# Performance work log

Hardware: AMD Instinct MI355X
Metric: run time of the kernel (lower is better)

## Reference

```python
import jax, jax.numpy as jnp
import numpy as np

B, F, S, H = 1024, 64, 512, 128


def setup_inputs() -> dict:
    key = jax.random.key(0)
    ks = jax.random.split(key, 9)
    x = jax.random.normal(ks[0], (B, F, S), dtype=jnp.float32)
    available_len = jax.random.randint(ks[1], (B,), 1, S // 2).astype(jnp.int32)
    extra = jax.random.randint(ks[2], (B,), 0, S // 2)
    predict_len = jnp.minimum(available_len + extra, S).astype(jnp.int32)
    s = 1.0 / float(np.sqrt(H))  # PyTorch default uniform init scale
    u = lambda k, shape: jax.random.uniform(k, shape, jnp.float32, -s, s)
    W_ih = u(ks[3], (4 * H, F))
    W_hh = u(ks[4], (4 * H, H))
    b_ih = u(ks[5], (4 * H,))
    b_hh = u(ks[6], (4 * H,))
    W_den = u(ks[7], (F, H))
    b_den = u(ks[8], (F,))
    init_ch = jnp.zeros((1, 2 * H), dtype=jnp.float32)  # nn.Parameter(zeros(1, 2*n_hidden))
    return {"x": x, "available_len": available_len, "predict_len": predict_len,
            "W_ih": W_ih, "W_hh": W_hh, "b_ih": b_ih, "b_hh": b_hh,
            "W_den": W_den, "b_den": b_den, "init_ch": init_ch}


def reference(x, available_len, predict_len, W_ih, W_hh, b_ih, b_hh, W_den, b_den, init_ch):
    """Masked autoregressive LSTMCell recurrence.

    Row r is active at step t iff t < predict_len[r]; once inactive it never
    re-activates (the torch code's per-step gather of c_1/h_1 by predict_len is
    exactly this monotone-shrinking active set, expressed here as a masked
    full-batch state update). For t >= available_len[r] (and still active) the
    input is the model's own previous prediction (auto-regression feedback).
    Returns the permuted buffer (seq_len, batch, n_fea), matching the torch code.
    """
    Bb, Ff, Ss = x.shape
    Hh = W_hh.shape[1]
    xs = jnp.transpose(x, (2, 0, 1))  # (S, B, F)
    c0 = jnp.broadcast_to(init_ch[:, :Hh], (Bb, Hh))
    h0 = jnp.broadcast_to(init_ch[:, Hh:], (Bb, Hh))

    def step(carry, inp):
        h, c, prev_out = carry
        t, x_t = inp  # t: scalar step index, x_t: (B, F)
        sel = t < predict_len                       # active rows
        use_pred = (t >= available_len) & sel
        inp_t = jnp.where(use_pred[:, None], prev_out, x_t)
        gates = inp_t @ W_ih.T + b_ih + h @ W_hh.T + b_hh  # (B, 4H)
        i, f, g, o = jnp.split(gates, 4, axis=-1)
        c_new = jax.nn.sigmoid(f) * c + jax.nn.sigmoid(i) * jnp.tanh(g)
        h_new = jax.nn.sigmoid(o) * jnp.tanh(c_new)
        h = jnp.where(sel[:, None], h_new, h)
        c = jnp.where(sel[:, None], c_new, c)
        pred = h_new @ W_den.T + b_den              # (B, F)
        out_t = jnp.where(sel[:, None], pred, inp_t)  # x[t, sel] <- prediction
        return (h, c, out_t), out_t

    _, ys = jax.lax.scan(step, (h0, c0, jnp.zeros_like(xs[0])),
                         (jnp.arange(Ss), xs))
    return ys  # (S, B, F)
```

## Files before the change

### kernel.cpp

```cpp
#include <hip/hip_runtime.h>

#define BB 1024
#define FF 64
#define SS 512
#define HH 128
#define ZP 200
#define ZROWS 16
#define OUTSTRIDE (BB*FF)

typedef __attribute__((ext_vector_type(8))) short bf16x8;
typedef __attribute__((ext_vector_type(4))) float f32x4;

__device__ __forceinline__ unsigned short f2bf(float f) {
    unsigned int u = __float_as_uint(f);
    u += 0x7fff + ((u >> 16) & 1);
    return (unsigned short)(u >> 16);
}

__device__ __forceinline__ void bar_lds() {
    asm volatile("s_waitcnt lgkmcnt(0)" ::: "memory");
    __builtin_amdgcn_s_barrier();
    __builtin_amdgcn_sched_barrier(0);
}

__global__ __launch_bounds__(512)
void lstm_mfma_kernel(const float* __restrict__ x,
                      const int* __restrict__ available_len,
                      const int* __restrict__ predict_len,
                      const float* __restrict__ W_ih,
                      const float* __restrict__ W_hh,
                      const float* __restrict__ b_ih,
                      const float* __restrict__ b_hh,
                      const float* __restrict__ W_den,
                      const float* __restrict__ b_den,
                      const float* __restrict__ init_ch,
                      float* __restrict__ out)
{
    const int b0  = blockIdx.x * 4;
    const int tid = threadIdx.x;
    const int w   = tid >> 6;
    const int l   = tid & 63;
    const int l16 = l & 15;
    const int lq  = l >> 4;
    const bool w4 = (w < 4);

    __shared__ __align__(16) unsigned short zbuf[2][ZROWS * ZP];

    for (int i = tid; i < 2 * ZROWS * ZP / 2; i += 512)
        ((unsigned int*)zbuf)[i] = 0u;

    const int p0 = predict_len[b0], p1 = predict_len[b0+1],
              p2 = predict_len[b0+2], p3 = predict_len[b0+3];
    const int maxP  = max(max(p0, p1), max(p2, p3));
    const int P_my  = predict_len[b0 + lq];
    const int AV_my = available_len[b0 + lq];

    bf16x8 wg[4][6];
    float bias[4];
    #pragma unroll
    for (int g = 0; g < 4; ++g) {
        const int n = 128*g + 16*w + l16;
        const float* rih = W_ih + n * FF;
        const float* rhh = W_hh + n * HH;
        #pragma unroll
        for (int kt = 0; kt < 6; ++kt) {
            const int k = 32*kt + 8*lq;
            const float* src = (k < 64) ? (rih + k) : (rhh + (k - 64));
            bf16x8 r;
            #pragma unroll
            for (int i = 0; i < 8; i++) r[i] = (short)f2bf(src[i]);
            wg[g][kt] = r;
        }
        bias[g] = b_ih[n] + b_hh[n];
    }

    bf16x8 wd0, wd1, wd2, wd3;
    float bden = 0.f;
    size_t xbase = 0;
    int AV_x = 0;
    if (w4) {
        const int f = 16*w + l16;
        const float* rd = W_den + f * HH;
        bf16x8 r;
        #pragma unroll
        for (int i = 0; i < 8; i++) r[i] = (short)f2bf(rd[0*32 + 8*lq + i]);
        wd0 = r;
        #pragma unroll
        for (int i = 0; i < 8; i++) r[i] = (short)f2bf(rd[1*32 + 8*lq + i]);
        wd1 = r;
        #pragma unroll
        for (int i = 0; i < 8; i++) r[i] = (short)f2bf(rd[2*32 + 8*lq + i]);
        wd2 = r;
        #pragma unroll
        for (int i = 0; i < 8; i++) r[i] = (short)f2bf(rd[3*32 + 8*lq + i]);
        wd3 = r;
        bden = b_den[f];
        xbase = ((size_t)(b0 + w) * FF + l) * SS;
        AV_x  = available_len[b0 + w];
    }

    const int unit  = 16*w + l16;
    const int abase = l16*ZP + 8*lq;
    float c = init_ch[unit];
    const float h0v = init_ch[HH + unit];
    float* outb = out + (size_t)(b0 + lq) * FF + 16*w + l16;

    bar_lds();

    zbuf[0][(4*lq)*ZP + 64 + unit] = f2bf(h0v);
    if (w4) zbuf[0][(4*w)*ZP + l] = f2bf(x[xbase]);

    float4 qc = {0.f,0.f,0.f,0.f};
    if (w4 && AV_x > 1) qc = *(const float4*)(x + xbase);

    int cur = 0;

#define DO_STEP(S, XNEXT)                                                      \
  do {                                                                         \
    const int s_ = (S);                                                        \
    bar_lds();                                               \
    const unsigned short* zc_ = zbuf[cur];                                     \
    bf16x8 a0 = *(const bf16x8*)(zc_ + abase +   0);                           \
    bf16x8 a1 = *(const bf16x8*)(zc_ + abase +  32);                           \
    bf16x8 a2 = *(const bf16x8*)(zc_ + abase +  64);                           \
    bf16x8 a3 = *(const bf16x8*)(zc_ + abase +  96);                           \
    bf16x8 a4 = *(const bf16x8*)(zc_ + abase + 128);                           \
    bf16x8 a5 = *(const bf16x8*)(zc_ + abase + 160);                           \
    f32x4 ac0 = {0.f,0.f,0.f,0.f}, ac1 = {0.f,0.f,0.f,0.f},                    \
          ac2 = {0.f,0.f,0.f,0.f}, ac3 = {0.f,0.f,0.f,0.f};                    \
    ac0 = __builtin_amdgcn_mfma_f32_16x16x32_bf16(a0, wg[0][0], ac0, 0,0,0);   \
    ac1 = __builtin_amdgcn_mfma_f32_16x16x32_bf16(a0, wg[1][0], ac1, 0,0,0);   \
    ac2 = __builtin_amdgcn_mfma_f32_16x16x32_bf16(a0, wg[2][0], ac2, 0,0,0);   \
    ac3 = __builtin_amdgcn_mfma_f32_16x16x32_bf16(a0, wg[3][0], ac3, 0,0,0);   \
    ac0 = __builtin_amdgcn_mfma_f32_16x16x32_bf16(a1, wg[0][1], ac0, 0,0,0);   \
    ac1 = __builtin_amdgcn_mfma_f32_16x16x32_bf16(a1, wg[1][1], ac1, 0,0,0);   \
    ac2 = __builtin_amdgcn_mfma_f32_16x16x32_bf16(a1, wg[2][1], ac2, 0,0,0);   \
    ac3 = __builtin_amdgcn_mfma_f32_16x16x32_bf16(a1, wg[3][1], ac3, 0,0,0);   \
    ac0 = __builtin_amdgcn_mfma_f32_16x16x32_bf16(a2, wg[0][2], ac0, 0,0,0);   \
    ac1 = __builtin_amdgcn_mfma_f32_16x16x32_bf16(a2, wg[1][2], ac1, 0,0,0);   \
    ac2 = __builtin_amdgcn_mfma_f32_16x16x32_bf16(a2, wg[2][2], ac2, 0,0,0);   \
    ac3 = __builtin_amdgcn_mfma_f32_16x16x32_bf16(a2, wg[3][2], ac3, 0,0,0);   \
    ac0 = __builtin_amdgcn_mfma_f32_16x16x32_bf16(a3, wg[0][3], ac0, 0,0,0);   \
    ac1 = __builtin_amdgcn_mfma_f32_16x16x32_bf16(a3, wg[1][3], ac1, 0,0,0);   \
    ac2 = __builtin_amdgcn_mfma_f32_16x16x32_bf16(a3, wg[2][3], ac2, 0,0,0);   \
    ac3 = __builtin_amdgcn_mfma_f32_16x16x32_bf16(a3, wg[3][3], ac3, 0,0,0);   \
    ac0 = __builtin_amdgcn_mfma_f32_16x16x32_bf16(a4, wg[0][4], ac0, 0,0,0);   \
    ac1 = __builtin_amdgcn_mfma_f32_16x16x32_bf16(a4, wg[1][4], ac1, 0,0,0);   \
    ac2 = __builtin_amdgcn_mfma_f32_16x16x32_bf16(a4, wg[2][4], ac2, 0,0,0);   \
    ac3 = __builtin_amdgcn_mfma_f32_16x16x32_bf16(a4, wg[3][4], ac3, 0,0,0);   \
    ac0 = __builtin_amdgcn_mfma_f32_16x16x32_bf16(a5, wg[0][5], ac0, 0,0,0);   \
    ac1 = __builtin_amdgcn_mfma_f32_16x16x32_bf16(a5, wg[1][5], ac1, 0,0,0);   \
    ac2 = __builtin_amdgcn_mfma_f32_16x16x32_bf16(a5, wg[2][5], ac2, 0,0,0);   \
    ac3 = __builtin_amdgcn_mfma_f32_16x16x32_bf16(a5, wg[3][5], ac3, 0,0,0);   \
    const float g0 = ac0[0] + bias[0];                                         \
    const float g1 = ac1[0] + bias[1];                                         \
    const float g2 = ac2[0] + bias[2];                                         \
    const float g3 = ac3[0] + bias[3];                                         \
    const float si = 1.f / (1.f + __expf(-g0));                                \
    const float sf = 1.f / (1.f + __expf(-g1));                                \
    const float tg = 1.f - 2.f / (__expf(2.f * g2) + 1.f);                     \
    const float so = 1.f / (1.f + __expf(-g3));                                \
    const float cn = sf * c + si * tg;                                         \
    const float tc = 1.f - 2.f / (__expf(2.f * cn) + 1.f);                     \
    const float hn = so * tc;                                                  \
    const int nxt_ = cur ^ 1;                                                  \
    if (s_ < P_my) { c = cn; zbuf[nxt_][(4*lq)*ZP + 64 + unit] = f2bf(hn); }   \
    bar_lds();                                                \
    if (w4) {                                                                  \
      const unsigned short* zn_ = zbuf[nxt_];                                  \
      bf16x8 h0f = *(const bf16x8*)(zn_ + abase + 64 +  0);                    \
      bf16x8 h1f = *(const bf16x8*)(zn_ + abase + 64 + 32);                    \
      bf16x8 h2f = *(const bf16x8*)(zn_ + abase + 64 + 64);                    \
      bf16x8 h3f = *(const bf16x8*)(zn_ + abase + 64 + 96);                    \
      f32x4 pa = {0.f,0.f,0.f,0.f}, pb = {0.f,0.f,0.f,0.f};                    \
      pa = __builtin_amdgcn_mfma_f32_16x16x32_bf16(h0f, wd0, pa, 0,0,0);       \
      pb = __builtin_amdgcn_mfma_f32_16x16x32_bf16(h2f, wd2, pb, 0,0,0);       \
      pa = __builtin_amdgcn_mfma_f32_16x16x32_bf16(h1f, wd1, pa, 0,0,0);       \
      pb = __builtin_amdgcn_mfma_f32_16x16x32_bf16(h3f, wd3, pb, 0,0,0);       \
      const float pred_ = pa[0] + pb[0] + bden;                                \
      if (s_ < P_my) {                                                         \
        outb[(size_t)s_ * OUTSTRIDE] = pred_;                                  \
        if (s_ + 1 >= AV_my)                                                   \
          zbuf[nxt_][(4*lq)*ZP + 16*w + l16] = f2bf(pred_);                    \
      }                                                                        \
      if (s_ + 1 < AV_x) zbuf[nxt_][(4*w)*ZP + l] = f2bf(XNEXT);               \
    }                                                                          \
    cur = nxt_;                                                                \
  } while (0)

    int t4 = 0;
    for (; t4 + 4 <= maxP; t4 += 4) {
        float4 qn = {0.f,0.f,0.f,0.f};
        if (w4 && (t4 + 4 < AV_x))
            qn = *(const float4*)(x + xbase + t4 + 4);
        DO_STEP(t4 + 0, qc.y);
        DO_STEP(t4 + 1, qc.z);
        DO_STEP(t4 + 2, qc.w);
        DO_STEP(t4 + 3, qn.x);
        qc = qn;
    }
    for (; t4 < maxP; ++t4) {
        float xs = 0.f;
        if (w4 && (t4 + 1 < AV_x)) xs = x[xbase + t4 + 1];
        DO_STEP(t4, xs);
    }
#undef DO_STEP
}

__global__ void tail_copy(const float* __restrict__ x,
                          const int* __restrict__ predict_len,
                          float* __restrict__ out)
{
    __shared__ float tile[64][65];
    const int b  = blockIdx.x;
    const int t0 = blockIdx.y * 64;
    const int P  = predict_len[b];
    if (t0 + 64 <= P) return;

    const int tid = threadIdx.x;
    const int tt  = tid & 63;
    const int fb  = tid >> 6;
    #pragma unroll
    for (int i = 0; i < 16; i++) {
        int f = fb * 16 + i;
        tile[f][tt] = x[(size_t)b * FF * SS + (size_t)f * SS + t0 + tt];
    }
    __syncthreads();
    const int f2 = tid & 63;
    const int tb = tid >> 6;
    #pragma unroll
    for (int i = 0; i < 16; i++) {
        int tloc = tb * 16 + i;
        int t    = t0 + tloc;
        if (t >= P) out[(size_t)t * BB * FF + (size_t)b * FF + f2] = tile[f2][tloc];
    }
}

extern "C" void kernel_launch(void* const* d_in, const int* in_sizes, int n_in,
                              void* d_out, int out_size, void* d_ws, size_t ws_size,
                              hipStream_t stream) {
    const float* x       = (const float*)d_in[0];
    const int*   avail   = (const int*)  d_in[1];
    const int*   plen    = (const int*)  d_in[2];
    const float* W_ih    = (const float*)d_in[3];
    const float* W_hh    = (const float*)d_in[4];
    const float* b_ih    = (const float*)d_in[5];
    const float* b_hh    = (const float*)d_in[6];
    const float* W_den   = (const float*)d_in[7];
    const float* b_den   = (const float*)d_in[8];
    const float* init_ch = (const float*)d_in[9];
    float*       out     = (float*)d_out;

    tail_copy<<<dim3(BB, SS/64), dim3(256), 0, stream>>>(x, plen, out);
    lstm_mfma_kernel<<<dim3(BB/4), dim3(512), 0, stream>>>(
        x, avail, plen, W_ih, W_hh, b_ih, b_hh, W_den, b_den, init_ch, out);
}
```

Baseline: 487.5 us.

## Pack 16 batch rows per block to fill MFMA M dimension

Each block now processes 16 batch rows instead of 4, so all four accumulator rows of every 16x16 MFMA tile carry useful data instead of zero padding. The cell update, predictions and x staging loop over four rows per lane, and every wave now loads x for two rows. The launch shrinks to a quarter of the blocks, which leaves most CUs idle. Each serial step also does four times the elementwise work, which may lengthen the latency-bound recurrence.

```diff
diff --git a/kernel.cpp b/kernel.cpp
--- a/kernel.cpp
+++ b/kernel.cpp
@@ -5,8 +5,7 @@
 #define SS 512
 #define HH 128
 #define ZP 200
-#define ZROWS 16
-#define OUTSTRIDE (BB*FF)
+#define OUTS (BB*FF)
 
 typedef __attribute__((ext_vector_type(8))) short bf16x8;
 typedef __attribute__((ext_vector_type(4))) float f32x4;
@@ -36,7 +35,7 @@
                       const float* __restrict__ init_ch,
                       float* __restrict__ out)
 {
-    const int b0  = blockIdx.x * 4;
+    const int b0  = blockIdx.x * 16;
     const int tid = threadIdx.x;
     const int w   = tid >> 6;
     const int l   = tid & 63;
@@ -44,16 +43,21 @@
     const int lq  = l >> 4;
     const bool w4 = (w < 4);
 
-    __shared__ __align__(16) unsigned short zbuf[2][ZROWS * ZP];
-
-    for (int i = tid; i < 2 * ZROWS * ZP / 2; i += 512)
+    __shared__ __align__(16) unsigned short zbuf[2][16 * ZP];
+
+    for (int i = tid; i < 2 * 16 * ZP / 2; i += 512)
         ((unsigned int*)zbuf)[i] = 0u;
 
-    const int p0 = predict_len[b0], p1 = predict_len[b0+1],
-              p2 = predict_len[b0+2], p3 = predict_len[b0+3];
-    const int maxP  = max(max(p0, p1), max(p2, p3));
-    const int P_my  = predict_len[b0 + lq];
-    const int AV_my = available_len[b0 + lq];
+    int maxP = 1;
+    #pragma unroll
+    for (int i = 0; i < 16; i++) maxP = max(maxP, predict_len[b0 + i]);
+
+    int Pv[4], Av[4];
+    #pragma unroll
+    for (int r = 0; r < 4; r++) {
+        Pv[r] = predict_len[b0 + 4*lq + r];
+        Av[r] = available_len[b0 + 4*lq + r];
+    }
 
     bf16x8 wg[4][6];
     float bias[4];
@@ -76,8 +80,6 @@
 
     bf16x8 wd0, wd1, wd2, wd3;
     float bden = 0.f;
-    size_t xbase = 0;
-    int AV_x = 0;
     if (w4) {
         const int f = 16*w + l16;
         const float* rd = W_den + f * HH;
@@ -95,30 +97,39 @@
         for (int i = 0; i < 8; i++) r[i] = (short)f2bf(rd[3*32 + 8*lq + i]);
         wd3 = r;
         bden = b_den[f];
-        xbase = ((size_t)(b0 + w) * FF + l) * SS;
-        AV_x  = available_len[b0 + w];
-    }
+    }
+
+    const size_t xb1 = ((size_t)(b0 + w)     * FF + l) * SS;
+    const size_t xb2 = ((size_t)(b0 + w + 8) * FF + l) * SS;
+    const int AX1 = available_len[b0 + w];
+    const int AX2 = available_len[b0 + w + 8];
 
     const int unit  = 16*w + l16;
     const int abase = l16*ZP + 8*lq;
-    float c = init_ch[unit];
-    const float h0v = init_ch[HH + unit];
-    float* outb = out + (size_t)(b0 + lq) * FF + 16*w + l16;
+    float cc[4];
+    const float c0v = init_ch[unit];
+    #pragma unroll
+    for (int r = 0; r < 4; r++) cc[r] = c0v;
+    const unsigned short h0b = f2bf(init_ch[HH + unit]);
+    float* outp = out + (size_t)(b0 + 4*lq) * FF + 16*w + l16;
 
     bar_lds();
 
-    zbuf[0][(4*lq)*ZP + 64 + unit] = f2bf(h0v);
-    if (w4) zbuf[0][(4*w)*ZP + l] = f2bf(x[xbase]);
-
-    float4 qc = {0.f,0.f,0.f,0.f};
-    if (w4 && AV_x > 1) qc = *(const float4*)(x + xbase);
+    #pragma unroll
+    for (int r = 0; r < 4; r++) zbuf[0][(4*lq + r)*ZP + 64 + unit] = h0b;
+    zbuf[0][w*ZP + l]       = f2bf(x[xb1]);
+    zbuf[0][(w + 8)*ZP + l] = f2bf(x[xb2]);
+
+    float4 q1 = {0.f,0.f,0.f,0.f}, q2 = {0.f,0.f,0.f,0.f};
+    if (AX1 > 1) q1 = *(const float4*)(x + xb1);
+    if (AX2 > 1) q2 = *(const float4*)(x + xb2);
 
     int cur = 0;
 
-#define DO_STEP(S, XNEXT)                                                      \
+#define DO_STEP(S, XN1, XN2)                                                   \
   do {                                                                         \
     const int s_ = (S);                                                        \
-    bar_lds();                                               \
+    bar_lds();                                                         \
     const unsigned short* zc_ = zbuf[cur];                                     \
     bf16x8 a0 = *(const bf16x8*)(zc_ + abase +   0);                           \
     bf16x8 a1 = *(const bf16x8*)(zc_ + abase +  32);                           \
@@ -152,19 +163,27 @@
     ac1 = __builtin_amdgcn_mfma_f32_16x16x32_bf16(a5, wg[1][5], ac1, 0,0,0);   \
     ac2 = __builtin_amdgcn_mfma_f32_16x16x32_bf16(a5, wg[2][5], ac2, 0,0,0);   \
     ac3 = __builtin_amdgcn_mfma_f32_16x16x32_bf16(a5, wg[3][5], ac3, 0,0,0);   \
-    const float g0 = ac0[0] + bias[0];                                         \
-    const float g1 = ac1[0] + bias[1];                                         \
-    const float g2 = ac2[0] + bias[2];                                         \
-    const float g3 = ac3[0] + bias[3];                                         \
-    const float si = 1.f / (1.f + __expf(-g0));                                \
-    const float sf = 1.f / (1.f + __expf(-g1));                                \
-    const float tg = 1.f - 2.f / (__expf(2.f * g2) + 1.f);                     \
-    const float so = 1.f / (1.f + __expf(-g3));                                \
-    const float cn = sf * c + si * tg;                                         \
-    const float tc = 1.f - 2.f / (__expf(2.f * cn) + 1.f);                     \
-    const float hn = so * tc;                                                  \
     const int nxt_ = cur ^ 1;                                                  \
-    if (s_ < P_my) { c = cn; zbuf[nxt_][(4*lq)*ZP + 64 + unit] = f2bf(hn); }   \
+    _Pragma("unroll")                                                          \
+    for (int r = 0; r < 4; r++) {                                              \
+      const float g0 = ac0[r] + bias[0];                                       \
+      const float g1 = ac1[r] + bias[1];                                       \
+      const float g2 = ac2[r] + bias[2];                                       \
+      const float g3 = ac3[r] + bias[3];                                       \
+      const float si = 1.f / (1.f + __expf(-g0));                              \
+      const float sf = 1.f / (1.f + __expf(-g1));                              \
+      const float tg = 1.f - 2.f / (__expf(2.f * g2) + 1.f);                   \
+      const float so = 1.f / (1.f + __expf(-g3));                              \
+      const float cn = sf * cc[r] + si * tg;                                   \
+      const float tc = 1.f - 2.f / (__expf(2.f * cn) + 1.f);                   \
+      const float hn = so * tc;                                                \
+      if (s_ < Pv[r]) {                                                        \
+        cc[r] = cn;                                                            \
+        zbuf[nxt_][(4*lq + r)*ZP + 64 + unit] = f2bf(hn);                      \
+      }                                                                        \
+    }                                                                          \
+    if (s_ + 1 < AX1) zbuf[nxt_][w*ZP + l]       = f2bf(XN1);                  \
+    if (s_ + 1 < AX2) zbuf[nxt_][(w + 8)*ZP + l] = f2bf(XN2);                  \
     bar_lds();                                                \
     if (w4) {                                                                  \
       const unsigned short* zn_ = zbuf[nxt_];                                  \
@@ -177,32 +196,35 @@
       pb = __builtin_amdgcn_mfma_f32_16x16x32_bf16(h2f, wd2, pb, 0,0,0);       \
       pa = __builtin_amdgcn_mfma_f32_16x16x32_bf16(h1f, wd1, pa, 0,0,0);       \
       pb = __builtin_amdgcn_mfma_f32_16x16x32_bf16(h3f, wd3, pb, 0,0,0);       \
-      const float pred_ = pa[0] + pb[0] + bden;                                \
-      if (s_ < P_my) {                                                         \
-        outb[(size_t)s_ * OUTSTRIDE] = pred_;                                  \
-        if (s_ + 1 >= AV_my)                                                   \
-          zbuf[nxt_][(4*lq)*ZP + 16*w + l16] = f2bf(pred_);                    \
+      _Pragma("unroll")                                                        \
+      for (int r = 0; r < 4; r++) {                                            \
+        if (s_ < Pv[r]) {                                                      \
+          const float pred_ = pa[r] + pb[r] + bden;                            \
+          outp[(size_t)s_ * OUTS + r * FF] = pred_;                            \
+          if (s_ + 1 >= Av[r])                                                 \
+            zbuf[nxt_][(4*lq + r)*ZP + 16*w + l16] = f2bf(pred_);              \
+        }                                                                      \
       }                                                                        \
-      if (s_ + 1 < AV_x) zbuf[nxt_][(4*w)*ZP + l] = f2bf(XNEXT);               \
     }                                                                          \
     cur = nxt_;                                                                \
   } while (0)
 
     int t4 = 0;
     for (; t4 + 4 <= maxP; t4 += 4) {
-        float4 qn = {0.f,0.f,0.f,0.f};
-        if (w4 && (t4 + 4 < AV_x))
-            qn = *(const float4*)(x + xbase + t4 + 4);
-        DO_STEP(t4 + 0, qc.y);
-        DO_STEP(t4 + 1, qc.z);
-        DO_STEP(t4 + 2, qc.w);
-        DO_STEP(t4 + 3, qn.x);
-        qc = qn;
+        float4 qn1 = {0.f,0.f,0.f,0.f}, qn2 = {0.f,0.f,0.f,0.f};
+        if (t4 + 4 < AX1) qn1 = *(const float4*)(x + xb1 + t4 + 4);
+        if (t4 + 4 < AX2) qn2 = *(const float4*)(x + xb2 + t4 + 4);
+        DO_STEP(t4 + 0, q1.y, q2.y);
+        DO_STEP(t4 + 1, q1.z, q2.z);
+        DO_STEP(t4 + 2, q1.w, q2.w);
+        DO_STEP(t4 + 3, qn1.x, qn2.x);
+        q1 = qn1; q2 = qn2;
     }
     for (; t4 < maxP; ++t4) {
-        float xs = 0.f;
-        if (w4 && (t4 + 1 < AV_x)) xs = x[xbase + t4 + 1];
-        DO_STEP(t4, xs);
+        float xs1 = 0.f, xs2 = 0.f;
+        if (t4 + 1 < AX1) xs1 = x[xb1 + t4 + 1];
+        if (t4 + 1 < AX2) xs2 = x[xb2 + t4 + 1];
+        DO_STEP(t4, xs1, xs2);
     }
 #undef DO_STEP
 }
@@ -252,6 +274,6 @@
     float*       out     = (float*)d_out;
 
     tail_copy<<<dim3(BB, SS/64), dim3(256), 0, stream>>>(x, plen, out);
-    lstm_mfma_kernel<<<dim3(BB/4), dim3(512), 0, stream>>>(
+    lstm_mfma_kernel<<<dim3(BB/16), dim3(512), 0, stream>>>(
         x, avail, plen, W_ih, W_hh, b_ih, b_hh, W_den, b_den, init_ch, out);
 }
```

Result: slower. 963.0 us (+97.5%).

## Fold dense output layer into recurrent weights for all-autoregressive tail steps

Applied to the files above, without the earlier changes.

Adds a pre-kernel that computes W_ih·W_den and W_ih·b_den into workspace. Once every row in a block is past its available length (t ≥ max available_len), the main kernel switches to a loop where the input contribution is folded into W_hh, so each step does a K=128 matmul instead of K=192. That loop also drops the per-step dependency on the prediction write-back through LDS, and computes the dense output off the critical path for the previous step. The barrier helper is reorganized with extra sched barriers. The trade-offs are an extra small kernel launch, a one-time weight reload, and changed bf16 rounding, because the folded weights are summed before quantization.

```diff
diff --git a/kernel.cpp b/kernel.cpp
--- a/kernel.cpp
+++ b/kernel.cpp
@@ -6,7 +6,7 @@
 #define HH 128
 #define ZP 200
 #define ZROWS 16
-#define OUTSTRIDE (BB*FF)
+#define OUTS (BB*FF)
 
 typedef __attribute__((ext_vector_type(8))) short bf16x8;
 typedef __attribute__((ext_vector_type(4))) float f32x4;
@@ -18,9 +18,28 @@
 }
 
 __device__ __forceinline__ void bar_lds() {
-    asm volatile("s_waitcnt lgkmcnt(0)" ::: "memory");
-    __builtin_amdgcn_s_barrier();
     __builtin_amdgcn_sched_barrier(0);
+    asm volatile("s_waitcnt lgkmcnt(0)\n\ts_barrier" ::: "memory");
+    __builtin_amdgcn_sched_barrier(0);
+}
+
+__global__ void fold_kernel(const float* __restrict__ W_ih,
+                            const float* __restrict__ W_den,
+                            const float* __restrict__ b_den,
+                            float* __restrict__ ws)
+{
+    const int n = blockIdx.x;
+    const int k = threadIdx.x;
+    float s = 0.f;
+    #pragma unroll 8
+    for (int f = 0; f < FF; ++f) s = fmaf(W_ih[n*FF + f], W_den[f*HH + k], s);
+    ws[n*HH + k] = s;
+    if (k == 0) {
+        float bsum = 0.f;
+        #pragma unroll 8
+        for (int f = 0; f < FF; ++f) bsum = fmaf(W_ih[n*FF + f], b_den[f], bsum);
+        ws[4*HH*HH + n] = bsum;
+    }
 }
 
 __global__ __launch_bounds__(512)
@@ -34,6 +53,7 @@
                       const float* __restrict__ W_den,
                       const float* __restrict__ b_den,
                       const float* __restrict__ init_ch,
+                      const float* __restrict__ ws,
                       float* __restrict__ out)
 {
     const int b0  = blockIdx.x * 4;
@@ -51,7 +71,10 @@
 
     const int p0 = predict_len[b0], p1 = predict_len[b0+1],
               p2 = predict_len[b0+2], p3 = predict_len[b0+3];
+    const int a0i = available_len[b0], a1i = available_len[b0+1],
+              a2i = available_len[b0+2], a3i = available_len[b0+3];
     const int maxP  = max(max(p0, p1), max(p2, p3));
+    const int tsw   = max(max(a0i, a1i), max(a2i, a3i));
     const int P_my  = predict_len[b0 + lq];
     const int AV_my = available_len[b0 + lq];
 
@@ -179,7 +202,7 @@
       pb = __builtin_amdgcn_mfma_f32_16x16x32_bf16(h3f, wd3, pb, 0,0,0);       \
       const float pred_ = pa[0] + pb[0] + bden;                                \
       if (s_ < P_my) {                                                         \
-        outb[(size_t)s_ * OUTSTRIDE] = pred_;                                  \
+        outb[(size_t)s_ * OUTS] = pred_;                                       \
         if (s_ + 1 >= AV_my)                                                   \
           zbuf[nxt_][(4*lq)*ZP + 16*w + l16] = f2bf(pred_);                    \
       }                                                                        \
@@ -189,7 +212,7 @@
   } while (0)
 
     int t4 = 0;
-    for (; t4 + 4 <= maxP; t4 += 4) {
+    for (; t4 + 4 <= tsw; t4 += 4) {
         float4 qn = {0.f,0.f,0.f,0.f};
         if (w4 && (t4 + 4 < AV_x))
             qn = *(const float4*)(x + xbase + t4 + 4);
@@ -199,12 +222,102 @@
         DO_STEP(t4 + 3, qn.x);
         qc = qn;
     }
-    for (; t4 < maxP; ++t4) {
+    for (; t4 < tsw; ++t4) {
         float xs = 0.f;
         if (w4 && (t4 + 1 < AV_x)) xs = x[xbase + t4 + 1];
         DO_STEP(t4, xs);
     }
 #undef DO_STEP
+
+    if (tsw < maxP) {
+        const float* wfold = ws;
+        const float* bfold = ws + 4*HH*HH;
+        #pragma unroll
+        for (int g = 0; g < 4; ++g) {
+            const int n = 128*g + 16*w + l16;
+            const float* rhh = W_hh + n * HH;
+            const float* rfo = wfold + n * HH;
+            #pragma unroll
+            for (int j = 0; j < 4; ++j) {
+                const int k = 32*j + 8*lq;
+                bf16x8 r;
+                #pragma unroll
+                for (int i = 0; i < 8; i++) r[i] = (short)f2bf(rhh[k+i] + rfo[k+i]);
+                wg[g][j] = r;
+            }
+            bias[g] += bfold[n];
+        }
+
+        for (int t = tsw; t < maxP; ++t) {
+            bar_lds();
+            const unsigned short* zc = zbuf[cur];
+            bf16x8 h0f = *(const bf16x8*)(zc + abase + 64 +  0);
+            bf16x8 h1f = *(const bf16x8*)(zc + abase + 64 + 32);
+            bf16x8 h2f = *(const bf16x8*)(zc + abase + 64 + 64);
+            bf16x8 h3f = *(const bf16x8*)(zc + abase + 64 + 96);
+
+            if (w4) {
+                f32x4 pa = {0.f,0.f,0.f,0.f}, pb = {0.f,0.f,0.f,0.f};
+                pa = __builtin_amdgcn_mfma_f32_16x16x32_bf16(h0f, wd0, pa, 0,0,0);
+                pb = __builtin_amdgcn_mfma_f32_16x16x32_bf16(h2f, wd2, pb, 0,0,0);
+                pa = __builtin_amdgcn_mfma_f32_16x16x32_bf16(h1f, wd1, pa, 0,0,0);
+                pb = __builtin_amdgcn_mfma_f32_16x16x32_bf16(h3f, wd3, pb, 0,0,0);
+                if (t > tsw && (t - 1) < P_my)
+                    outb[(size_t)(t-1) * OUTS] = pa[0] + pb[0] + bden;
+            }
+
+            f32x4 ac0 = {0.f,0.f,0.f,0.f}, ac1 = {0.f,0.f,0.f,0.f},
+                  ac2 = {0.f,0.f,0.f,0.f}, ac3 = {0.f,0.f,0.f,0.f};
+            ac0 = __builtin_amdgcn_mfma_f32_16x16x32_bf16(h0f, wg[0][0], ac0, 0,0,0);
+            ac1 = __builtin_amdgcn_mfma_f32_16x16x32_bf16(h0f, wg[1][0], ac1, 0,0,0);
+            ac2 = __builtin_amdgcn_mfma_f32_16x16x32_bf16(h0f, wg[2][0], ac2, 0,0,0);
+            ac3 = __builtin_amdgcn_mfma_f32_16x16x32_bf16(h0f, wg[3][0], ac3, 0,0,0);
+            ac0 = __builtin_amdgcn_mfma_f32_16x16x32_bf16(h1f, wg[0][1], ac0, 0,0,0);
+            ac1 = __builtin_amdgcn_mfma_f32_16x16x32_bf16(h1f, wg[1][1], ac1, 0,0,0);
+            ac2 = __builtin_amdgcn_mfma_f32_16x16x32_bf16(h1f, wg[2][1], ac2, 0,0,0);
+            ac3 = __builtin_amdgcn_mfma_f32_16x16x32_bf16(h1f, wg[3][1], ac3, 0,0,0);
+            ac0 = __builtin_amdgcn_mfma_f32_16x16x32_bf16(h2f, wg[0][2], ac0, 0,0,0);
+            ac1 = __builtin_amdgcn_mfma_f32_16x16x32_bf16(h2f, wg[1][2], ac1, 0,0,0);
+            ac2 = __builtin_amdgcn_mfma_f32_16x16x32_bf16(h2f, wg[2][2], ac2, 0,0,0);
+            ac3 = __builtin_amdgcn_mfma_f32_16x16x32_bf16(h2f, wg[3][2], ac3, 0,0,0);
+            ac0 = __builtin_amdgcn_mfma_f32_16x16x32_bf16(h3f, wg[0][3], ac0, 0,0,0);
+            ac1 = __builtin_amdgcn_mfma_f32_16x16x32_bf16(h3f, wg[1][3], ac1, 0,0,0);
+            ac2 = __builtin_amdgcn_mfma_f32_16x16x32_bf16(h3f, wg[2][3], ac2, 0,0,0);
+            ac3 = __builtin_amdgcn_mfma_f32_16x16x32_bf16(h3f, wg[3][3], ac3, 0,0,0);
+
+            const float g0 = ac0[0] + bias[0];
+            const float g1 = ac1[0] + bias[1];
+            const float g2 = ac2[0] + bias[2];
+            const float g3 = ac3[0] + bias[3];
+            const float si = 1.f / (1.f + __expf(-g0));
+            const float sf = 1.f / (1.f + __expf(-g1));
+            const float tg = 1.f - 2.f / (__expf(2.f * g2) + 1.f);
+            const float so = 1.f / (1.f + __expf(-g3));
+            const float cn = sf * c + si * tg;
+            const float tc = 1.f - 2.f / (__expf(2.f * cn) + 1.f);
+            const float hn = so * tc;
+
+            const int nxt = cur ^ 1;
+            if (t < P_my) { c = cn; zbuf[nxt][(4*lq)*ZP + 64 + unit] = f2bf(hn); }
+            cur = nxt;
+        }
+
+        bar_lds();
+        if (w4) {
+            const unsigned short* zc = zbuf[cur];
+            bf16x8 h0f = *(const bf16x8*)(zc + abase + 64 +  0);
+            bf16x8 h1f = *(const bf16x8*)(zc + abase + 64 + 32);
+            bf16x8 h2f = *(const bf16x8*)(zc + abase + 64 + 64);
+            bf16x8 h3f = *(const bf16x8*)(zc + abase + 64 + 96);
+            f32x4 pa = {0.f,0.f,0.f,0.f}, pb = {0.f,0.f,0.f,0.f};
+            pa = __builtin_amdgcn_mfma_f32_16x16x32_bf16(h0f, wd0, pa, 0,0,0);
+            pb = __builtin_amdgcn_mfma_f32_16x16x32_bf16(h2f, wd2, pb, 0,0,0);
+            pa = __builtin_amdgcn_mfma_f32_16x16x32_bf16(h1f, wd1, pa, 0,0,0);
+            pb = __builtin_amdgcn_mfma_f32_16x16x32_bf16(h3f, wd3, pb, 0,0,0);
+            if ((maxP - 1) < P_my)
+                outb[(size_t)(maxP-1) * OUTS] = pa[0] + pb[0] + bden;
+        }
+    }
 }
 
 __global__ void tail_copy(const float* __restrict__ x,
@@ -250,8 +363,10 @@
     const float* b_den   = (const float*)d_in[8];
     const float* init_ch = (const float*)d_in[9];
     float*       out     = (float*)d_out;
-
+    float*       ws      = (float*)d_ws;
+
+    fold_kernel<<<dim3(4*HH), dim3(HH), 0, stream>>>(W_ih, W_den, b_den, ws);
     tail_copy<<<dim3(BB, SS/64), dim3(256), 0, stream>>>(x, plen, out);
     lstm_mfma_kernel<<<dim3(BB/4), dim3(512), 0, stream>>>(
-        x, avail, plen, W_ih, W_hh, b_ih, b_hh, W_den, b_den, init_ch, out);
-}
+        x, avail, plen, W_ih, W_hh, b_ih, b_hh, W_den, b_den, init_ch, ws, out);
+}
```

Result: faster. 444.9 us (-8.7%).
